# Kernel tuning notes

Hardware: AMD Instinct MI355X
Metric: run time of the kernel (lower is better)

## Reference

```python
import jax, jax.numpy as jnp
import numpy as np

B, S, D, U = 32, 2048, 1024, 1024


def setup_inputs() -> dict:
    key = jax.random.key(0)
    ks = jax.random.split(key, 8)
    scale_in = 1.0 / np.sqrt(D)
    scale_u = 1.0 / np.sqrt(U)
    return {
        "query": jax.random.normal(ks[0], (B, D), dtype=jnp.float32),
        "values": jax.random.normal(ks[1], (B, S, D), dtype=jnp.float32),
        "W1": jax.random.normal(ks[2], (D, U), dtype=jnp.float32) * scale_in,
        "b1": jnp.zeros((U,), dtype=jnp.float32),
        "W2": jax.random.normal(ks[3], (D, U), dtype=jnp.float32) * scale_in,
        "b2": jnp.zeros((U,), dtype=jnp.float32),
        "V": jax.random.normal(ks[4], (U, 1), dtype=jnp.float32) * scale_u,
        "bV": jnp.zeros((1,), dtype=jnp.float32),
    }


def reference(query, values, W1, b1, W2, b2, V, bV):
    # values: [B, S, D] -> [B, S, U]; query: [B, D] -> [B, 1, U]
    proj_v = jnp.einsum("bsd,du->bsu", values, W1) + b1
    proj_q = (query @ W2 + b2)[:, None, :]
    # score: [B, S, 1]
    score = jnp.einsum("bsu,uo->bso", jnp.tanh(proj_v + proj_q), V) + bV
    attention_weights = jax.nn.softmax(score, axis=1)
    # context: [B, D]
    context_vector = jnp.sum(attention_weights * values, axis=1)
    return (context_vector, attention_weights)
```

## Files before the change

### kernel.cpp

```cpp
#include <hip/hip_runtime.h>

#define DEVFN __device__ __forceinline__

typedef __attribute__((ext_vector_type(4))) float f32x4;
typedef __attribute__((ext_vector_type(8))) short short8;
typedef __attribute__((ext_vector_type(4))) unsigned int uint4v;
typedef __attribute__((ext_vector_type(8))) unsigned short ushort8;

constexpr int CB = 32;
constexpr int CS = 2048;
constexpr int CD = 1024;
constexpr int CU = 1024;
constexpr int CM = CB * CS;

DEVFN unsigned f2bf_u(float f) {
    unsigned u = __float_as_uint(f);
    return (u + 0x7FFFu + ((u >> 16) & 1u)) >> 16;
}
DEVFN unsigned f2bf_pack(float lo, float hi) {
    return f2bf_u(lo) | (f2bf_u(hi) << 16);
}
DEVFN short8 cvt8(f32x4 a, f32x4 b) {
    uint4v p;
    p[0] = f2bf_pack(a[0], a[1]);
    p[1] = f2bf_pack(a[2], a[3]);
    p[2] = f2bf_pack(b[0], b[1]);
    p[3] = f2bf_pack(b[2], b[3]);
    return __builtin_bit_cast(short8, p);
}
DEVFN float tanh_fast(float x) {
    float e = exp2f(x * 2.885390081777927f);
    return 1.0f - 2.0f * __builtin_amdgcn_rcpf(e + 1.0f);
}

__global__ void k_bias1(const float* __restrict__ q, const float* __restrict__ W2,
                        float* __restrict__ bpart) {
    int dc = blockIdx.x, b = blockIdx.y;
    int t = threadIdx.x;
    __shared__ float qs[128];
    if (t < 128) qs[t] = q[b * CD + dc * 128 + t];
    __syncthreads();
    float acc0 = 0.f, acc1 = 0.f, acc2 = 0.f, acc3 = 0.f;
    const float* w2 = W2 + (size_t)(dc * 128) * CU + t;
#pragma unroll 4
    for (int d = 0; d < 128; ++d) {
        float qv = qs[d];
        const float* r = w2 + (size_t)d * CU;
        acc0 += qv * r[0];
        acc1 += qv * r[256];
        acc2 += qv * r[512];
        acc3 += qv * r[768];
    }
    float* o = bpart + (size_t)(b * 8 + dc) * CU + t;
    o[0] = acc0; o[256] = acc1; o[512] = acc2; o[768] = acc3;
}

__global__ void k_bias2(const float* __restrict__ bpart, const float* __restrict__ b1,
                        const float* __restrict__ b2, float* __restrict__ bias) {
    int idx = blockIdx.x * 256 + threadIdx.x;
    int b = idx >> 10, u = idx & 1023;
    float s = b1[u] + b2[u];
#pragma unroll
    for (int dc = 0; dc < 8; ++dc) s += bpart[(size_t)(b * 8 + dc) * CU + u];
    bias[idx] = s;
}

__global__ void k_packW1(const float* __restrict__ W1, unsigned short* __restrict__ W1p) {
    int tid = blockIdx.x * 256 + threadIdx.x;
    int o8  = tid * 8;
    int l   = (o8 >> 3) & 63;
    int ub  = (o8 >> 9) & 15;
    int ut  = (o8 >> 13) & 3;
    int kt  = o8 >> 15;
    int u  = ut * 256 + ub * 16 + (l & 15);
    int d0 = kt * 32 + (l >> 4) * 8;
    ushort8 v;
#pragma unroll
    for (int j = 0; j < 8; ++j)
        v[j] = (unsigned short)f2bf_u(W1[(size_t)(d0 + j) * CU + u]);
    *(ushort8*)(W1p + o8) = v;
}

__global__ __launch_bounds__(512, 2) void k_score(
    const float* __restrict__ values, const unsigned short* __restrict__ W1p,
    const float* __restrict__ bias, const float* __restrict__ V,
    float* __restrict__ score2) {
    __shared__ __align__(16) char smem[24576];

    const int t = threadIdx.x;
    const int w = t >> 6, l = t & 63;
    const int p = blockIdx.x;
    const int xt = (p & 7) + (p >> 4) * 8;
    const int uc = (p >> 3) & 1;
    const int ph = xt & 31;
    const int m0 = xt * 128;
    const int bb = m0 >> 11;

    const float* aSrc = values + (size_t)(m0 + (t >> 2)) * CD + (t & 3) * 8;
    const int llw = (l >> 2) | ((l & 3) << 4);
    const int aWr = w * 1024 + ((llw ^ (((llw >> 4) & 3) << 1)) << 4);
    const int aRd = (l ^ (((l >> 4) & 3) << 1)) << 4;
    const unsigned short* bBase = W1p + (size_t)(uc * 2 + (w >> 2)) * 8192
                                + (w & 3) * 2048 + l * 8;

    f32x4 acc[8][4];
#pragma unroll
    for (int i = 0; i < 8; ++i)
#pragma unroll
        for (int j = 0; j < 4; ++j) acc[i][j] = f32x4{0.f, 0.f, 0.f, 0.f};

    short8 bF0[4], bF1[4];
    f32x4 pXa, pXb, pYa, pYb;
    char* ldsR = (char*)smem;
    char* ldsW = (char*)smem + 16384;

    {
        const int k0 = ph, k1 = (ph + 1) & 31, k2 = (ph + 2) & 31;
        const unsigned short* bs = bBase + (size_t)k0 * 32768;
#pragma unroll
        for (int jj = 0; jj < 4; ++jj)
            bF0[jj] = *(const short8*)(bs + jj * 512);
        pXa = *(const f32x4*)(aSrc + k0 * 32);
        pXb = *(const f32x4*)(aSrc + k0 * 32 + 4);
        pYa = *(const f32x4*)(aSrc + k1 * 32);
        pYb = *(const f32x4*)(aSrc + k1 * 32 + 4);
        *(short8*)(smem + aWr) = cvt8(pXa, pXb);
        *(short8*)(smem + 8192 + aWr) = cvt8(pYa, pYb);
        pYa = *(const f32x4*)(aSrc + k2 * 32);
        pYb = *(const f32x4*)(aSrc + k2 * 32 + 4);
        asm volatile("s_waitcnt lgkmcnt(0)" ::: "memory");
        asm volatile("s_barrier" ::: "memory");
    }

#define SCORE_BODY(KT, BFC, BFN, PWa, PWb, PLa, PLb, DO_LDB, DO_LDA, DO_WR)         \
    {                                                                               \
        asm volatile("s_waitcnt lgkmcnt(1)" ::: "memory");                          \
        asm volatile("s_barrier" ::: "memory");                                     \
        if (DO_LDB) {                                                               \
            const int kp = ((KT) + 1 + ph) & 31;                                    \
            const unsigned short* bs = bBase + (size_t)kp * 32768;                  \
            _Pragma("unroll")                                                       \
            for (int jj = 0; jj < 4; ++jj)                                          \
                BFN[jj] = *(const short8*)(bs + jj * 512);                          \
        }                                                                           \
        if (DO_LDA) {                                                               \
            const int kp = ((KT) + 3 + ph) & 31;                                    \
            PLa = *(const f32x4*)(aSrc + kp * 32);                                  \
            PLb = *(const f32x4*)(aSrc + kp * 32 + 4);                              \
        }                                                                           \
        short8 aF[8];                                                               \
        _Pragma("unroll")                                                           \
        for (int i = 0; i < 8; ++i)                                                 \
            aF[i] = *(const short8*)(ldsR + i * 1024 + aRd);                        \
        __builtin_amdgcn_s_setprio(1);                                              \
        _Pragma("unroll")                                                           \
        for (int i = 0; i < 8; ++i)                                                 \
            _Pragma("unroll")                                                       \
            for (int j = 0; j < 4; ++j)                                             \
                acc[i][j] = __builtin_amdgcn_mfma_f32_16x16x32_bf16(                \
                    aF[i], BFC[j], acc[i][j], 0, 0, 0);                             \
        __builtin_amdgcn_s_setprio(0);                                              \
        if (DO_WR)                                                                  \
            *(short8*)(ldsW + aWr) = cvt8(PWa, PWb);                                \
        ldsW = ldsR;                                                                \
        ldsR = (ldsR == (char*)smem + 16384) ? (char*)smem : ldsR + 8192;           \
    }

    for (int kt = 0; kt < 28; kt += 2) {
        SCORE_BODY(kt,     bF0, bF1, pYa, pYb, pXa, pXb, 1, 1, 1)
        SCORE_BODY(kt + 1, bF1, bF0, pXa, pXb, pYa, pYb, 1, 1, 1)
    }
    SCORE_BODY(28, bF0, bF1, pYa, pYb, pXa, pXb, 1, 1, 1)
    SCORE_BODY(29, bF1, bF0, pXa, pXb, pYa, pYb, 1, 0, 1)
    SCORE_BODY(30, bF0, bF1, pYa, pYb, pXa, pXb, 1, 0, 0)
    SCORE_BODY(31, bF1, bF0, pXa, pXb, pYa, pYb, 0, 0, 0)
#undef SCORE_BODY

    float part[8][4];
#pragma unroll
    for (int i = 0; i < 8; ++i)
#pragma unroll
        for (int rr = 0; rr < 4; ++rr) part[i][rr] = 0.f;

#pragma unroll
    for (int j = 0; j < 4; ++j) {
        const int col = uc * 512 + w * 64 + j * 16 + (l & 15);
        const float vv = V[col];
        const float bz = bias[bb * CU + col];
#pragma unroll
        for (int i = 0; i < 8; ++i)
#pragma unroll
            for (int rr = 0; rr < 4; ++rr)
                part[i][rr] += vv * tanh_fast(acc[i][j][rr] + bz);
    }

    __syncthreads();
    float* red = (float*)smem;
#pragma unroll
    for (int i = 0; i < 8; ++i)
#pragma unroll
        for (int rr = 0; rr < 4; ++rr) {
            float v = part[i][rr];
            v += __shfl_xor(v, 1);
            v += __shfl_xor(v, 2);
            v += __shfl_xor(v, 4);
            v += __shfl_xor(v, 8);
            if ((l & 15) == 0)
                red[w * 128 + i * 16 + (l >> 4) * 4 + rr] = v;
        }
    __syncthreads();
    if (t < 128) {
        float sv = 0.f;
#pragma unroll
        for (int ww = 0; ww < 8; ++ww) sv += red[ww * 128 + t];
        score2[(size_t)uc * CM + m0 + t] = sv;
    }
}

__global__ void k_softmax(const float* __restrict__ score2, float* __restrict__ wts) {
    int b = blockIdx.x, t = threadIdx.x;
    int i0 = b * CS + t, i1 = i0 + 1024;
    float s0 = score2[i0] + score2[CM + i0];
    float s1 = score2[i1] + score2[CM + i1];
    __shared__ float red[16];
    int wv = t >> 6, ln = t & 63;
    float m = fmaxf(s0, s1);
#pragma unroll
    for (int o = 32; o >= 1; o >>= 1) m = fmaxf(m, __shfl_xor(m, o));
    if (ln == 0) red[wv] = m;
    __syncthreads();
    float M = red[0];
#pragma unroll
    for (int k = 1; k < 16; ++k) M = fmaxf(M, red[k]);
    float e0 = __expf(s0 - M), e1 = __expf(s1 - M);
    float sm = e0 + e1;
#pragma unroll
    for (int o = 32; o >= 1; o >>= 1) sm += __shfl_xor(sm, o);
    __syncthreads();
    if (ln == 0) red[wv] = sm;
    __syncthreads();
    float T = 0.f;
#pragma unroll
    for (int k = 0; k < 16; ++k) T += red[k];
    float inv = 1.0f / T;
    wts[i0] = e0 * inv;
    wts[i1] = e1 * inv;
}

__global__ void k_ctx_part(const float* __restrict__ values, const float* __restrict__ wts,
                           float* __restrict__ part) {
    int b = blockIdx.y, sc = blockIdx.x;
    int t = threadIdx.x;
    const float* vb = values + ((size_t)b * CS + sc * 64) * CD + t * 4;
    const float* wb = wts + b * CS + sc * 64;
    f32x4 a = {0.f, 0.f, 0.f, 0.f};
#pragma unroll 8
    for (int s = 0; s < 64; ++s) {
        float wgt = wb[s];
        f32x4 v = *(const f32x4*)(vb + (size_t)s * CD);
        a += v * wgt;
    }
    *(f32x4*)(part + (size_t)(b * 32 + sc) * CD + t * 4) = a;
}

__global__ void k_ctx_red(const float* __restrict__ part, float* __restrict__ ctx) {
    int idx = blockIdx.x * 256 + threadIdx.x;
    int b = idx >> 10, d = idx & 1023;
    float s = 0.f;
#pragma unroll 8
    for (int c = 0; c < 32; ++c) s += part[(size_t)(b * 32 + c) * CD + d];
    ctx[idx] = s;
}

extern "C" void kernel_launch(void* const* d_in, const int* in_sizes, int n_in,
                              void* d_out, int out_size, void* d_ws, size_t ws_size,
                              hipStream_t stream) {
    const float* query  = (const float*)d_in[0];
    const float* values = (const float*)d_in[1];
    const float* W1     = (const float*)d_in[2];
    const float* b1     = (const float*)d_in[3];
    const float* W2     = (const float*)d_in[4];
    const float* b2     = (const float*)d_in[5];
    const float* V      = (const float*)d_in[6];

    float* out = (float*)d_out;
    float* ctx = out;
    float* wts = out + 32768;

    char* ws = (char*)d_ws;
    float*          score2 = (float*)ws;
    float*          bias   = (float*)(ws + (1 << 20));
    unsigned short* W1p    = (unsigned short*)(ws + (1 << 20) + (1 << 17));
    float*          part   = (float*)(ws + (1 << 20) + (1 << 17) + (1 << 21));
    float*          bpart  = part;

    k_bias1<<<dim3(8, 32), 256, 0, stream>>>(query, W2, bpart);
    k_bias2<<<128, 256, 0, stream>>>(bpart, b1, b2, bias);
    k_packW1<<<512, 256, 0, stream>>>(W1, W1p);
    k_score<<<1024, 512, 0, stream>>>(values, W1p, bias, V, score2);
    k_softmax<<<32, 1024, 0, stream>>>(score2, wts);
    k_ctx_part<<<dim3(32, 32), 256, 0, stream>>>(values, wts, part);
    k_ctx_red<<<128, 256, 0, stream>>>(part, ctx);
}
```

Before: 220.5 us.

## Split score GEMM into four 256-column blocks with XCD-aware tile mapping

The score kernel now uses 256-thread blocks, each covering 256 of the U columns, instead of 512-thread blocks covering 512 columns. The grid doubles to 2048 blocks, and the softmax kernel now sums four partial scores instead of two. A new block-to-tile mapping places the four column chunks of the same row tile on the same XCD, at adjacent launch positions, so the values tile can be shared through L2. The aim is smaller blocks that give more scheduling flexibility and occupancy. The cost is that each values tile is now loaded and converted to bf16 four times instead of twice, and more partial-score traffic is written and read.

```diff
diff --git a/kernel.cpp b/kernel.cpp
--- a/kernel.cpp
+++ b/kernel.cpp
@@ -81,27 +81,30 @@
     *(ushort8*)(W1p + o8) = v;
 }
 
-__global__ __launch_bounds__(512, 2) void k_score(
+__global__ __launch_bounds__(256, 2) void k_score(
     const float* __restrict__ values, const unsigned short* __restrict__ W1p,
     const float* __restrict__ bias, const float* __restrict__ V,
-    float* __restrict__ score2) {
+    float* __restrict__ score4) {
     __shared__ __align__(16) char smem[24576];
 
     const int t = threadIdx.x;
     const int w = t >> 6, l = t & 63;
     const int p = blockIdx.x;
-    const int xt = (p & 7) + (p >> 4) * 8;
-    const int uc = (p >> 3) & 1;
+    const int L = (p & 7) * 256 + (p >> 3);
+    const int xt = L >> 2;
+    const int uc = L & 3;
     const int ph = xt & 31;
     const int m0 = xt * 128;
     const int bb = m0 >> 11;
 
-    const float* aSrc = values + (size_t)(m0 + (t >> 2)) * CD + (t & 3) * 8;
-    const int llw = (l >> 2) | ((l & 3) << 4);
-    const int aWr = w * 1024 + ((llw ^ (((llw >> 4) & 3) << 1)) << 4);
+    const int sRow = t >> 1, sH = t & 1;
+    const float* aSrcT = values + (size_t)(m0 + sRow) * CD + sH * 16;
+    const int c0 = sH * 2, c1 = sH * 2 + 1;
+    const int ll0 = (sRow & 15) | (c0 << 4), ll1 = (sRow & 15) | (c1 << 4);
+    const int aWr0 = (sRow >> 4) * 1024 + ((ll0 ^ (((ll0 >> 4) & 3) << 1)) << 4);
+    const int aWr1 = (sRow >> 4) * 1024 + ((ll1 ^ (((ll1 >> 4) & 3) << 1)) << 4);
     const int aRd = (l ^ (((l >> 4) & 3) << 1)) << 4;
-    const unsigned short* bBase = W1p + (size_t)(uc * 2 + (w >> 2)) * 8192
-                                + (w & 3) * 2048 + l * 8;
+    const unsigned short* bBase = W1p + (size_t)uc * 8192 + w * 2048 + l * 8;
 
     f32x4 acc[8][4];
 #pragma unroll
@@ -110,7 +113,7 @@
         for (int j = 0; j < 4; ++j) acc[i][j] = f32x4{0.f, 0.f, 0.f, 0.f};
 
     short8 bF0[4], bF1[4];
-    f32x4 pXa, pXb, pYa, pYb;
+    f32x4 hX0, hX1, hX2, hX3, hY0, hY1, hY2, hY3;
     char* ldsR = (char*)smem;
     char* ldsW = (char*)smem + 16384;
 
@@ -120,21 +123,33 @@
 #pragma unroll
         for (int jj = 0; jj < 4; ++jj)
             bF0[jj] = *(const short8*)(bs + jj * 512);
-        pXa = *(const f32x4*)(aSrc + k0 * 32);
-        pXb = *(const f32x4*)(aSrc + k0 * 32 + 4);
-        pYa = *(const f32x4*)(aSrc + k1 * 32);
-        pYb = *(const f32x4*)(aSrc + k1 * 32 + 4);
-        *(short8*)(smem + aWr) = cvt8(pXa, pXb);
-        *(short8*)(smem + 8192 + aWr) = cvt8(pYa, pYb);
-        pYa = *(const f32x4*)(aSrc + k2 * 32);
-        pYb = *(const f32x4*)(aSrc + k2 * 32 + 4);
+        const float* ap = aSrcT + k0 * 32;
+        hX0 = *(const f32x4*)(ap);
+        hX1 = *(const f32x4*)(ap + 4);
+        hX2 = *(const f32x4*)(ap + 8);
+        hX3 = *(const f32x4*)(ap + 12);
+        *(short8*)(smem + aWr0) = cvt8(hX0, hX1);
+        *(short8*)(smem + aWr1) = cvt8(hX2, hX3);
+        const float* ap1 = aSrcT + k1 * 32;
+        hX0 = *(const f32x4*)(ap1);
+        hX1 = *(const f32x4*)(ap1 + 4);
+        hX2 = *(const f32x4*)(ap1 + 8);
+        hX3 = *(const f32x4*)(ap1 + 12);
+        *(short8*)(smem + 8192 + aWr0) = cvt8(hX0, hX1);
+        *(short8*)(smem + 8192 + aWr1) = cvt8(hX2, hX3);
+        const float* ap2 = aSrcT + k2 * 32;
+        hX0 = *(const f32x4*)(ap2);
+        hX1 = *(const f32x4*)(ap2 + 4);
+        hX2 = *(const f32x4*)(ap2 + 8);
+        hX3 = *(const f32x4*)(ap2 + 12);
         asm volatile("s_waitcnt lgkmcnt(0)" ::: "memory");
         asm volatile("s_barrier" ::: "memory");
     }
 
-#define SCORE_BODY(KT, BFC, BFN, PWa, PWb, PLa, PLb, DO_LDB, DO_LDA, DO_WR)         \
+#define SCORE_BODY(KT, BFC, BFN, PW0, PW1, PW2, PW3, PL0, PL1, PL2, PL3,            \
+                   DO_LDB, DO_LDA, DO_WR)                                           \
     {                                                                               \
-        asm volatile("s_waitcnt lgkmcnt(1)" ::: "memory");                          \
+        asm volatile("s_waitcnt lgkmcnt(2)" ::: "memory");                          \
         asm volatile("s_barrier" ::: "memory");                                     \
         if (DO_LDB) {                                                               \
             const int kp = ((KT) + 1 + ph) & 31;                                    \
@@ -145,8 +160,11 @@
         }                                                                           \
         if (DO_LDA) {                                                               \
             const int kp = ((KT) + 3 + ph) & 31;                                    \
-            PLa = *(const f32x4*)(aSrc + kp * 32);                                  \
-            PLb = *(const f32x4*)(aSrc + kp * 32 + 4);                              \
+            const float* ap = aSrcT + kp * 32;                                      \
+            PL0 = *(const f32x4*)(ap);                                              \
+            PL1 = *(const f32x4*)(ap + 4);                                          \
+            PL2 = *(const f32x4*)(ap + 8);                                          \
+            PL3 = *(const f32x4*)(ap + 12);                                         \
         }                                                                           \
         short8 aF[8];                                                               \
         _Pragma("unroll")                                                           \
@@ -160,20 +178,22 @@
                 acc[i][j] = __builtin_amdgcn_mfma_f32_16x16x32_bf16(                \
                     aF[i], BFC[j], acc[i][j], 0, 0, 0);                             \
         __builtin_amdgcn_s_setprio(0);                                              \
-        if (DO_WR)                                                                  \
-            *(short8*)(ldsW + aWr) = cvt8(PWa, PWb);                                \
+        if (DO_WR) {                                                                \
+            *(short8*)(ldsW + aWr0) = cvt8(PW0, PW1);                               \
+            *(short8*)(ldsW + aWr1) = cvt8(PW2, PW3);                               \
+        }                                                                           \
         ldsW = ldsR;                                                                \
         ldsR = (ldsR == (char*)smem + 16384) ? (char*)smem : ldsR + 8192;           \
     }
 
     for (int kt = 0; kt < 28; kt += 2) {
-        SCORE_BODY(kt,     bF0, bF1, pYa, pYb, pXa, pXb, 1, 1, 1)
-        SCORE_BODY(kt + 1, bF1, bF0, pXa, pXb, pYa, pYb, 1, 1, 1)
-    }
-    SCORE_BODY(28, bF0, bF1, pYa, pYb, pXa, pXb, 1, 1, 1)
-    SCORE_BODY(29, bF1, bF0, pXa, pXb, pYa, pYb, 1, 0, 1)
-    SCORE_BODY(30, bF0, bF1, pYa, pYb, pXa, pXb, 1, 0, 0)
-    SCORE_BODY(31, bF1, bF0, pXa, pXb, pYa, pYb, 0, 0, 0)
+        SCORE_BODY(kt,     bF0, bF1, hX0, hX1, hX2, hX3, hY0, hY1, hY2, hY3, 1, 1, 1)
+        SCORE_BODY(kt + 1, bF1, bF0, hY0, hY1, hY2, hY3, hX0, hX1, hX2, hX3, 1, 1, 1)
+    }
+    SCORE_BODY(28, bF0, bF1, hX0, hX1, hX2, hX3, hY0, hY1, hY2, hY3, 1, 1, 1)
+    SCORE_BODY(29, bF1, bF0, hY0, hY1, hY2, hY3, hX0, hX1, hX2, hX3, 1, 0, 1)
+    SCORE_BODY(30, bF0, bF1, hX0, hX1, hX2, hX3, hY0, hY1, hY2, hY3, 1, 0, 0)
+    SCORE_BODY(31, bF1, bF0, hY0, hY1, hY2, hY3, hX0, hX1, hX2, hX3, 0, 0, 0)
 #undef SCORE_BODY
 
     float part[8][4];
@@ -184,7 +204,7 @@
 
 #pragma unroll
     for (int j = 0; j < 4; ++j) {
-        const int col = uc * 512 + w * 64 + j * 16 + (l & 15);
+        const int col = uc * 256 + w * 64 + j * 16 + (l & 15);
         const float vv = V[col];
         const float bz = bias[bb * CU + col];
 #pragma unroll
@@ -210,18 +230,16 @@
         }
     __syncthreads();
     if (t < 128) {
-        float sv = 0.f;
-#pragma unroll
-        for (int ww = 0; ww < 8; ++ww) sv += red[ww * 128 + t];
-        score2[(size_t)uc * CM + m0 + t] = sv;
-    }
-}
-
-__global__ void k_softmax(const float* __restrict__ score2, float* __restrict__ wts) {
+        float sv = red[t] + red[128 + t] + red[256 + t] + red[384 + t];
+        score4[(size_t)uc * CM + m0 + t] = sv;
+    }
+}
+
+__global__ void k_softmax(const float* __restrict__ score4, float* __restrict__ wts) {
     int b = blockIdx.x, t = threadIdx.x;
     int i0 = b * CS + t, i1 = i0 + 1024;
-    float s0 = score2[i0] + score2[CM + i0];
-    float s1 = score2[i1] + score2[CM + i1];
+    float s0 = score4[i0] + score4[CM + i0] + score4[2 * CM + i0] + score4[3 * CM + i0];
+    float s1 = score4[i1] + score4[CM + i1] + score4[2 * CM + i1] + score4[3 * CM + i1];
     __shared__ float red[16];
     int wv = t >> 6, ln = t & 63;
     float m = fmaxf(s0, s1);
@@ -288,7 +306,7 @@
     float* wts = out + 32768;
 
     char* ws = (char*)d_ws;
-    float*          score2 = (float*)ws;
+    float*          score4 = (float*)ws;
     float*          bias   = (float*)(ws + (1 << 20));
     unsigned short* W1p    = (unsigned short*)(ws + (1 << 20) + (1 << 17));
     float*          part   = (float*)(ws + (1 << 20) + (1 << 17) + (1 << 21));
@@ -297,8 +315,8 @@
     k_bias1<<<dim3(8, 32), 256, 0, stream>>>(query, W2, bpart);
     k_bias2<<<128, 256, 0, stream>>>(bpart, b1, b2, bias);
     k_packW1<<<512, 256, 0, stream>>>(W1, W1p);
-    k_score<<<1024, 512, 0, stream>>>(values, W1p, bias, V, score2);
-    k_softmax<<<32, 1024, 0, stream>>>(score2, wts);
+    k_score<<<2048, 256, 0, stream>>>(values, W1p, bias, V, score4);
+    k_softmax<<<32, 1024, 0, stream>>>(score4, wts);
     k_ctx_part<<<dim3(32, 32), 256, 0, stream>>>(values, wts, part);
     k_ctx_red<<<128, 256, 0, stream>>>(part, ctx);
 }
```

Measured after the change: 231.0 us. 1.05x slower.

## Write bf16 copy of values during score pass and read it for context

Applied to the files above, without the earlier changes.

While staging values into LDS, the score kernel (uc==0 blocks) also streams the bf16-converted tiles to a workspace buffer with nontemporal stores. The context partial-sum kernel then reads this half-size bf16 copy instead of the fp32 values, cutting the second full pass over values roughly in half. This adds a 128MB write during the score kernel, and the context vector now uses bf16-rounded values, which loses some accuracy. The fp32 fallback path also switches to nontemporal loads.

```diff
diff --git a/kernel.cpp b/kernel.cpp
--- a/kernel.cpp
+++ b/kernel.cpp
@@ -6,6 +6,7 @@
 typedef __attribute__((ext_vector_type(8))) short short8;
 typedef __attribute__((ext_vector_type(4))) unsigned int uint4v;
 typedef __attribute__((ext_vector_type(8))) unsigned short ushort8;
+typedef __attribute__((ext_vector_type(4))) unsigned short ushort4v;
 
 constexpr int CB = 32;
 constexpr int CS = 2048;
@@ -84,7 +85,7 @@
 __global__ __launch_bounds__(512, 2) void k_score(
     const float* __restrict__ values, const unsigned short* __restrict__ W1p,
     const float* __restrict__ bias, const float* __restrict__ V,
-    float* __restrict__ score2) {
+    float* __restrict__ score2, unsigned short* __restrict__ valbf) {
     __shared__ __align__(16) char smem[24576];
 
     const int t = threadIdx.x;
@@ -95,8 +96,11 @@
     const int ph = xt & 31;
     const int m0 = xt * 128;
     const int bb = m0 >> 11;
+    const bool doVB = (valbf != nullptr) && (uc == 0);
 
     const float* aSrc = values + (size_t)(m0 + (t >> 2)) * CD + (t & 3) * 8;
+    unsigned short* vbT = valbf ? valbf + (size_t)(m0 + (t >> 2)) * CD + (t & 3) * 8
+                                : nullptr;
     const int llw = (l >> 2) | ((l & 3) << 4);
     const int aWr = w * 1024 + ((llw ^ (((llw >> 4) & 3) << 1)) << 4);
     const int aRd = (l ^ (((l >> 4) & 3) << 1)) << 4;
@@ -124,8 +128,14 @@
         pXb = *(const f32x4*)(aSrc + k0 * 32 + 4);
         pYa = *(const f32x4*)(aSrc + k1 * 32);
         pYb = *(const f32x4*)(aSrc + k1 * 32 + 4);
-        *(short8*)(smem + aWr) = cvt8(pXa, pXb);
-        *(short8*)(smem + 8192 + aWr) = cvt8(pYa, pYb);
+        short8 v0 = cvt8(pXa, pXb);
+        short8 v1 = cvt8(pYa, pYb);
+        *(short8*)(smem + aWr) = v0;
+        *(short8*)(smem + 8192 + aWr) = v1;
+        if (doVB) {
+            __builtin_nontemporal_store(v0, (short8*)(vbT + (size_t)k0 * 32));
+            __builtin_nontemporal_store(v1, (short8*)(vbT + (size_t)k1 * 32));
+        }
         pYa = *(const f32x4*)(aSrc + k2 * 32);
         pYb = *(const f32x4*)(aSrc + k2 * 32 + 4);
         asm volatile("s_waitcnt lgkmcnt(0)" ::: "memory");
@@ -160,8 +170,14 @@
                 acc[i][j] = __builtin_amdgcn_mfma_f32_16x16x32_bf16(                \
                     aF[i], BFC[j], acc[i][j], 0, 0, 0);                             \
         __builtin_amdgcn_s_setprio(0);                                              \
-        if (DO_WR)                                                                  \
-            *(short8*)(ldsW + aWr) = cvt8(PWa, PWb);                                \
+        if (DO_WR) {                                                                \
+            short8 vw = cvt8(PWa, PWb);                                             \
+            *(short8*)(ldsW + aWr) = vw;                                            \
+            if (doVB) {                                                             \
+                const int kw = ((KT) + 2 + ph) & 31;                                \
+                __builtin_nontemporal_store(vw, (short8*)(vbT + (size_t)kw * 32));  \
+            }                                                                       \
+        }                                                                           \
         ldsW = ldsR;                                                                \
         ldsR = (ldsR == (char*)smem + 16384) ? (char*)smem : ldsR + 8192;           \
     }
@@ -245,6 +261,24 @@
     float inv = 1.0f / T;
     wts[i0] = e0 * inv;
     wts[i1] = e1 * inv;
+}
+
+__global__ void k_ctx_part_bf(const unsigned short* __restrict__ valbf,
+                              const float* __restrict__ wts, float* __restrict__ part) {
+    int b = blockIdx.y, sc = blockIdx.x;
+    int t = threadIdx.x;
+    const unsigned short* vb = valbf + ((size_t)b * CS + sc * 64) * CD + t * 4;
+    const float* wb = wts + b * CS + sc * 64;
+    f32x4 a = {0.f, 0.f, 0.f, 0.f};
+#pragma unroll 8
+    for (int s = 0; s < 64; ++s) {
+        float wgt = wb[s];
+        ushort4v u = __builtin_nontemporal_load((const ushort4v*)(vb + (size_t)s * CD));
+#pragma unroll
+        for (int j = 0; j < 4; ++j)
+            a[j] += wgt * __uint_as_float((unsigned)u[j] << 16);
+    }
+    *(f32x4*)(part + (size_t)(b * 32 + sc) * CD + t * 4) = a;
 }
 
 __global__ void k_ctx_part(const float* __restrict__ values, const float* __restrict__ wts,
@@ -257,7 +291,7 @@
 #pragma unroll 8
     for (int s = 0; s < 64; ++s) {
         float wgt = wb[s];
-        f32x4 v = *(const f32x4*)(vb + (size_t)s * CD);
+        f32x4 v = __builtin_nontemporal_load((const f32x4*)(vb + (size_t)s * CD));
         a += v * wgt;
     }
     *(f32x4*)(part + (size_t)(b * 32 + sc) * CD + t * 4) = a;
@@ -294,11 +328,18 @@
     float*          part   = (float*)(ws + (1 << 20) + (1 << 17) + (1 << 21));
     float*          bpart  = part;
 
+    const size_t vbNeed = (size_t)(8u << 20) + (size_t)CM * CD * sizeof(unsigned short);
+    unsigned short* valbf = (ws_size >= vbNeed)
+                          ? (unsigned short*)(ws + (8u << 20)) : nullptr;
+
     k_bias1<<<dim3(8, 32), 256, 0, stream>>>(query, W2, bpart);
     k_bias2<<<128, 256, 0, stream>>>(bpart, b1, b2, bias);
     k_packW1<<<512, 256, 0, stream>>>(W1, W1p);
-    k_score<<<1024, 512, 0, stream>>>(values, W1p, bias, V, score2);
+    k_score<<<1024, 512, 0, stream>>>(values, W1p, bias, V, score2, valbf);
     k_softmax<<<32, 1024, 0, stream>>>(score2, wts);
-    k_ctx_part<<<dim3(32, 32), 256, 0, stream>>>(values, wts, part);
+    if (valbf)
+        k_ctx_part_bf<<<dim3(32, 32), 256, 0, stream>>>(valbf, wts, part);
+    else
+        k_ctx_part<<<dim3(32, 32), 256, 0, stream>>>(values, wts, part);
     k_ctx_red<<<128, 256, 0, stream>>>(part, ctx);
 }
```

Measured after the change: 262.1 us. +18.9%, slower.
